# Kernel tuning notes

Measured on AMD Instinct MI355X. Metric: run time of the kernel, lower is better.

Reference implementation:

```python
import jax, jax.numpy as jnp
import numpy as np

B = 1024          # batch
H = 512           # hidden_dim
T = 256           # seq_len
CD = 2            # coord_dim
LAT = 64 + 64 + 128  # total latent dim


def setup_inputs() -> dict:
    key = jax.random.key(0)
    ks = jax.random.split(key, 20)
    s = 0.05  # weight init scale
    rn = lambda k, shp: (jax.random.normal(k, shp, dtype=jnp.float32) * s)
    return {
        "z_primitive": jax.random.normal(ks[0], (B, 64), dtype=jnp.float32),
        "z_skill": jax.random.normal(ks[1], (B, 64), dtype=jnp.float32),
        "z_style": jax.random.normal(ks[2], (B, 128), dtype=jnp.float32),
        "W_proj": rn(ks[3], (2 * H, LAT)),
        "b_proj": jnp.zeros((2 * H,), jnp.float32),
        "Wih1": rn(ks[4], (4 * H, CD)),
        "Whh1": rn(ks[5], (4 * H, H)),
        "bih1": jnp.zeros((4 * H,), jnp.float32),
        "bhh1": jnp.zeros((4 * H,), jnp.float32),
        "Wih2": rn(ks[6], (4 * H, H)),
        "Whh2": rn(ks[7], (4 * H, H)),
        "bih2": jnp.zeros((4 * H,), jnp.float32),
        "bhh2": jnp.zeros((4 * H,), jnp.float32),
        "Wo1": rn(ks[8], (H // 2, H)),
        "bo1": jnp.zeros((H // 2,), jnp.float32),
        "Wo2": rn(ks[9], (CD, H // 2)),
        "bo2": jnp.zeros((CD,), jnp.float32),
    }


def _lstm_cell(x, h, c, Wih, Whh, bih, bhh):
    # PyTorch gate order: i, f, g, o
    gates = x @ Wih.T + h @ Whh.T + (bih + bhh)
    i, f, g, o = jnp.split(gates, 4, axis=1)
    c_new = jax.nn.sigmoid(f) * c + jax.nn.sigmoid(i) * jnp.tanh(g)
    h_new = jax.nn.sigmoid(o) * jnp.tanh(c_new)
    return h_new, c_new


def reference(z_primitive, z_skill, z_style, W_proj, b_proj,
              Wih1, Whh1, bih1, bhh1, Wih2, Whh2, bih2, bhh2,
              Wo1, bo1, Wo2, bo2):
    z = jnp.concatenate([z_primitive, z_skill, z_style], axis=1)  # [B, LAT]
    init = z @ W_proj.T + b_proj                                  # [B, 2H]
    h0 = init[:, :H]
    c0 = init[:, H:]
    x0 = jnp.zeros((z.shape[0], CD), init.dtype)

    def step(carry, _):
        x, h1, c1, h2, c2 = carry
        h1, c1 = _lstm_cell(x, h1, c1, Wih1, Whh1, bih1, bhh1)
        h2, c2 = _lstm_cell(h1, h2, c2, Wih2, Whh2, bih2, bhh2)
        # output MLP (Dropout inactive in eval)
        y = jax.nn.relu(h2 @ Wo1.T + bo1) @ Wo2.T + bo2  # [B, CD]
        return (y, h1, c1, h2, c2), y

    # h0/c0 repeated across both LSTM layers (repeat(2,1,1) in torch)
    _, ys = jax.lax.scan(step, (x0, h0, c0, h0, c0), None, length=T)
    return jnp.transpose(ys, (1, 0, 2))  # [B, T, CD]
```

## Files before the change

kernel.cpp:

```cpp
#include <hip/hip_runtime.h>
#include <math.h>

#define NB 1024
#define NH 512
#define NT 256
#define NCD 2

typedef unsigned short u16;
typedef __bf16 bf16x8 __attribute__((ext_vector_type(8)));
typedef float  f32x4  __attribute__((ext_vector_type(4)));

#define MFMA_BF16 __builtin_amdgcn_mfma_f32_16x16x32_bf16

__device__ __forceinline__ float sigf(float x) { return 1.0f / (1.0f + expf(-x)); }
__device__ __forceinline__ float b2f(u16 u) {
    union { unsigned i; float f; } v; v.i = ((unsigned)u) << 16; return v.f;
}
__device__ __forceinline__ u16 f2b(float f) {
    union { float f; unsigned i; } v; v.f = f;
    unsigned r = v.i + 0x7fffu + ((v.i >> 16) & 1u);
    return (u16)(r >> 16);
}

__device__ __forceinline__ void async_cp16(const void* gptr, void* lptr) {
    __builtin_amdgcn_global_load_lds(
        (const __attribute__((address_space(1))) unsigned int*)gptr,
        (__attribute__((address_space(3))) unsigned int*)lptr,
        16, 0, 0);
}

__global__ __launch_bounds__(256) void convert3(
    const float* __restrict__ a, const float* __restrict__ b,
    const float* __restrict__ c,
    u16* __restrict__ oa, u16* __restrict__ ob, u16* __restrict__ oc)
{
    const int i = blockIdx.x * 256 + threadIdx.x;
    oa[i] = f2b(a[i]); ob[i] = f2b(b[i]); oc[i] = f2b(c[i]);
}

__global__ __launch_bounds__(256) void convw1(
    const float* __restrict__ a, u16* __restrict__ o)
{
    const int i = blockIdx.x * 256 + threadIdx.x;
    o[i] = f2b(a[i]);
}

__global__ __launch_bounds__(256) void bsum_k(
    const float* __restrict__ bi1, const float* __restrict__ bh1,
    const float* __restrict__ bi2, const float* __restrict__ bh2,
    float* __restrict__ o1, float* __restrict__ o2)
{
    const int i = blockIdx.x * 256 + threadIdx.x;
    o1[i] = bi1[i] + bh1[i];
    o2[i] = bi2[i] + bh2[i];
}

__global__ __launch_bounds__(256) void init_kernel(
    const float* __restrict__ zp, const float* __restrict__ zs,
    const float* __restrict__ zst, const float* __restrict__ Wp,
    const float* __restrict__ bp,
    u16* __restrict__ h1, float* __restrict__ c1,
    u16* __restrict__ h2, float* __restrict__ c2)
{
    __shared__ float z[4][256];
    const int tid = threadIdx.x;
    const int b0  = blockIdx.x * 4;
    for (int i = tid; i < 4 * 256; i += 256) {
        const int bb = i >> 8, k = i & 255;
        float v;
        if (k < 64)       v = zp [(b0 + bb) * 64  + k];
        else if (k < 128) v = zs [(b0 + bb) * 64  + (k - 64)];
        else              v = zst[(b0 + bb) * 128 + (k - 128)];
        z[bb][k] = v;
    }
    __syncthreads();
    for (int rt = 0; rt < 4; ++rt) {
        const int r = rt * 256 + tid;
        const float bias = bp[r];
        float a0 = bias, a1 = bias, a2 = bias, a3 = bias;
        for (int k = 0; k < 256; ++k) {
            const float w = Wp[r * 256 + k];
            a0 += z[0][k] * w; a1 += z[1][k] * w;
            a2 += z[2][k] * w; a3 += z[3][k] * w;
        }
        const float acc[4] = {a0, a1, a2, a3};
        for (int bb = 0; bb < 4; ++bb) {
            const int b = b0 + bb;
            if (r < NH) {
                h1[b * NH + r] = f2b(acc[bb]);
                h2[b * NH + r] = f2b(acc[bb]);
            } else {
                c1[b * NH + r - NH] = acc[bb];
                c2[b * NH + r - NH] = acc[bb];
            }
        }
    }
}

__global__ __launch_bounds__(512, 4) void fused_out_lstm1(
    const u16* __restrict__ h2prev,
    const u16* __restrict__ A0,
    const u16* __restrict__ W0,
    const float* __restrict__ bsum,
    const float* __restrict__ Wx,
    const u16* __restrict__ W1b,
    const float* __restrict__ bo1, const float* __restrict__ Wo2,
    const float* __restrict__ bo2, float* __restrict__ outp,
    float* __restrict__ c, u16* __restrict__ hnext,
    const int t, const int do_lstm)
{
    __shared__ __align__(16) char smem[61440];
    float* eg  = (float*)smem;
    float* red = (float*)(smem + 36864);

    const int tid  = threadIdx.x;
    const int lane = tid & 63;
    const int wv   = tid >> 6;
    const int g    = wv & 3;
    const int mh   = wv >> 2;
    const int l15  = lane & 15;
    const int q    = lane >> 4;
    const int bx   = blockIdx.x;
    const int ut   = (bx & 7) * 2 + ((bx >> 3) & 1);
    const int grp  = bx >> 4;
    const int b0   = grp * 32;
    const int u0   = ut * 32;

    int goffW0, goffW1, goffA = 0, goffO[4];
    {
        const int c0 = (wv * 2) * 64 + lane;
        const int w0r = c0 >> 3;
        goffW0 = ((w0r >> 5) * NH + u0 + (w0r & 31)) * NH + (((c0 & 7) ^ (w0r & 7)) * 8);
        const int c1i = (wv * 2 + 1) * 64 + lane;
        const int w1r = c1i >> 3;
        goffW1 = ((w1r >> 5) * NH + u0 + (w1r & 31)) * NH + (((c1i & 7) ^ (w1r & 7)) * 8);
        if (wv < 4) {
            const int ca = wv * 64 + lane;
            const int ar = ca >> 3;
            goffA = (b0 + ar) * NH + (((ca & 7) ^ (ar & 7)) * 8);
        }
#pragma unroll
        for (int i = 0; i < 4; ++i) {
            const int cidx = (wv * 4 + i) * 64 + lane;
            const int row  = cidx >> 3;
            const int kc   = (cidx & 7) ^ (row & 7);
            goffO[i] = row * NH + kc * 8;
        }
    }

    auto issue = [&](int m, int bi) {
        const int k0 = (m & 7) * 64;
        char* base = smem + bi * 20480;
        async_cp16((const void*)(W0 + goffW0 + k0),
                   (void*)(base + 4096 + (wv * 2) * 1024));
        async_cp16((const void*)(W0 + goffW1 + k0),
                   (void*)(base + 4096 + (wv * 2 + 1) * 1024));
        if (wv < 4)
            async_cp16((const void*)(A0 + goffA + k0),
                       (void*)(base + wv * 1024));
    };

    const int u_e  = tid & 31;
    const int bq_e = tid >> 5;
    const int ug_e = u0 + u_e;
    float bs[4], wx0[4], wx1[4], cpre[2];
#pragma unroll
    for (int g4 = 0; g4 < 4; ++g4) bs[g4] = bsum[g4 * NH + ug_e];
#pragma unroll
    for (int g4 = 0; g4 < 4; ++g4) {
        wx0[g4] = Wx[(g4 * NH + ug_e) * 2 + 0];
        wx1[g4] = Wx[(g4 * NH + ug_e) * 2 + 1];
    }
    cpre[0] = c[(size_t)(b0 + bq_e * 2 + 0) * NH + ug_e];
    cpre[1] = c[(size_t)(b0 + bq_e * 2 + 1) * NH + ug_e];

    if (do_lstm) issue(0, 2);

    float r_x[4] = {0.f, 0.f, 0.f, 0.f};

    if (h2prev) {
        f32x4 acc_o[2][2];
#pragma unroll
        for (int mi = 0; mi < 2; ++mi)
#pragma unroll
            for (int ni = 0; ni < 2; ++ni)
                acc_o[mi][ni] = (f32x4){0.f, 0.f, 0.f, 0.f};

        for (int kk = 0; kk < 8; ++kk) {
            __syncthreads();
            const int k0 = kk * 64;
#pragma unroll
            for (int i = 0; i < 4; ++i)
                async_cp16((const void*)(W1b + goffO[i] + k0),
                           (void*)(smem + ((wv * 4 + i) << 10)));
            if (wv < 4)
                async_cp16((const void*)(h2prev + goffA + k0),
                           (void*)(smem + 32768 + (wv << 10)));
            asm volatile("s_waitcnt vmcnt(0)" ::: "memory");
            __builtin_amdgcn_s_barrier();
#pragma unroll
            for (int kh = 0; kh < 2; ++kh) {
                bf16x8 bfr[2], av[2];
#pragma unroll
                for (int ni = 0; ni < 2; ++ni) {
                    const int wrow = wv * 32 + ni * 16 + l15;
                    const int j = (kh * 4 + q) ^ (wrow & 7);
                    bfr[ni] = *(const bf16x8*)(smem + wrow * 128 + j * 16);
                }
#pragma unroll
                for (int mi = 0; mi < 2; ++mi) {
                    const int row = mi * 16 + l15;
                    const int j = (kh * 4 + q) ^ (row & 7);
                    av[mi] = *(const bf16x8*)(smem + 32768 + row * 128 + j * 16);
                }
#pragma unroll
                for (int mi = 0; mi < 2; ++mi)
#pragma unroll
                    for (int ni = 0; ni < 2; ++ni)
                        acc_o[mi][ni] = MFMA_BF16(av[mi], bfr[ni], acc_o[mi][ni], 0, 0, 0);
            }
        }
        float bo1n[2], w20[2], w21[2];
#pragma unroll
        for (int ni = 0; ni < 2; ++ni) {
            const int n = wv * 32 + ni * 16 + l15;
            bo1n[ni] = bo1[n]; w20[ni] = Wo2[n]; w21[ni] = Wo2[256 + n];
        }
        float pa[2][4], pb[2][4];
#pragma unroll
        for (int mi = 0; mi < 2; ++mi)
#pragma unroll
            for (int r = 0; r < 4; ++r) {
                const float s0 = fmaxf(acc_o[mi][0][r] + bo1n[0], 0.f);
                const float s1 = fmaxf(acc_o[mi][1][r] + bo1n[1], 0.f);
                pa[mi][r] = s0 * w20[0] + s1 * w20[1];
                pb[mi][r] = s0 * w21[0] + s1 * w21[1];
            }
#pragma unroll
        for (int off = 1; off < 16; off <<= 1)
#pragma unroll
            for (int mi = 0; mi < 2; ++mi)
#pragma unroll
                for (int r = 0; r < 4; ++r) {
                    pa[mi][r] += __shfl_xor(pa[mi][r], off, 64);
                    pb[mi][r] += __shfl_xor(pb[mi][r], off, 64);
                }
        if (l15 == 0) {
#pragma unroll
            for (int mi = 0; mi < 2; ++mi)
#pragma unroll
                for (int r = 0; r < 4; ++r) {
                    const int m = mi * 16 + q * 4 + r;
                    red[m * 16 + wv * 2 + 0] = pa[mi][r];
                    red[m * 16 + wv * 2 + 1] = pb[mi][r];
                }
        }
        __syncthreads();
        if (ut == 0 && tid < 64) {
            const int bl = tid >> 1, cc = tid & 1;
            float y = bo2[cc];
#pragma unroll
            for (int w8 = 0; w8 < 8; ++w8) y += red[bl * 16 + w8 * 2 + cc];
            outp[(size_t)(b0 + bl) * (NT * NCD) + (t - 1) * NCD + cc] = y;
        }
        if (do_lstm) {
            const int bq = tid >> 5;
#pragma unroll
            for (int jj = 0; jj < 2; ++jj)
#pragma unroll
                for (int cc = 0; cc < 2; ++cc) {
                    float y = bo2[cc];
#pragma unroll
                    for (int w8 = 0; w8 < 8; ++w8)
                        y += red[(bq * 2 + jj) * 16 + w8 * 2 + cc];
                    r_x[jj * 2 + cc] = y;
                }
        }
        __syncthreads();
    }
    if (!do_lstm) return;

    f32x4 acc[2];
    acc[0] = (f32x4){0.f, 0.f, 0.f, 0.f};
    acc[1] = (f32x4){0.f, 0.f, 0.f, 0.f};
    const int M = 8;
    issue(1, 0);
    int ci = 2;
    for (int m = 0; m < M; ++m) {
        if (m + 1 < M) {
            if (wv < 4) asm volatile("s_waitcnt vmcnt(3)" ::: "memory");
            else        asm volatile("s_waitcnt vmcnt(2)" ::: "memory");
        } else {
            asm volatile("s_waitcnt vmcnt(0)" ::: "memory");
        }
        __builtin_amdgcn_s_barrier();
        if (m + 2 < M) {
            int bi = ci + 2; if (bi >= 3) bi -= 3;
            issue(m + 2, bi);
        }
        const char* bA = smem + ci * 20480;
        const char* bW = bA + 4096;
#pragma unroll
        for (int khi = 0; khi < 2; ++khi) {
            bf16x8 bfr[2];
#pragma unroll
            for (int ni = 0; ni < 2; ++ni) {
                const int wrow = g * 32 + ni * 16 + l15;
                const int j = (khi * 4 + q) ^ (wrow & 7);
                bfr[ni] = *(const bf16x8*)(bW + wrow * 128 + j * 16);
            }
            const int row = mh * 16 + l15;
            const int j = (khi * 4 + q) ^ (row & 7);
            const bf16x8 av = *(const bf16x8*)(bA + row * 128 + j * 16);
            acc[0] = MFMA_BF16(av, bfr[0], acc[0], 0, 0, 0);
            acc[1] = MFMA_BF16(av, bfr[1], acc[1], 0, 0, 0);
        }
        ++ci; if (ci == 3) ci = 0;
    }

    __syncthreads();
#pragma unroll
    for (int ni = 0; ni < 2; ++ni)
#pragma unroll
        for (int r = 0; r < 4; ++r)
            eg[(g * 32 + mh * 16 + q * 4 + r) * 33 + ni * 16 + l15] = acc[ni][r];
    __syncthreads();

#pragma unroll
    for (int jj = 0; jj < 2; ++jj) {
        const int bl = bq_e * 2 + jj;
        const int b  = b0 + bl;
        float gv[4];
#pragma unroll
        for (int g4 = 0; g4 < 4; ++g4) gv[g4] = eg[(g4 * 32 + bl) * 33 + u_e] + bs[g4];
        const float x0 = r_x[jj * 2 + 0];
        const float x1 = r_x[jj * 2 + 1];
#pragma unroll
        for (int g4 = 0; g4 < 4; ++g4) gv[g4] += x0 * wx0[g4] + x1 * wx1[g4];
        const float iv = sigf(gv[0]);
        const float fv = sigf(gv[1]);
        const float gg = tanhf(gv[2]);
        const float ov = sigf(gv[3]);
        const size_t idx = (size_t)b * NH + ug_e;
        const float cn = fv * cpre[jj] + iv * gg;
        c[idx] = cn;
        hnext[idx] = f2b(ov * tanhf(cn));
    }
}

__global__ __launch_bounds__(512, 4) void lstm_mfma32(
    const u16* __restrict__ A0, const u16* __restrict__ W0,
    const u16* __restrict__ A1, const u16* __restrict__ W1,
    const float* __restrict__ bsum,
    float* __restrict__ c, u16* __restrict__ hnext,
    const int npass)
{
    __shared__ __align__(16) char smem[61440];
    float* eg = (float*)smem;

    const int tid  = threadIdx.x;
    const int lane = tid & 63;
    const int wv   = tid >> 6;
    const int g    = wv & 3;
    const int mh   = wv >> 2;
    const int l15  = lane & 15;
    const int q    = lane >> 4;
    const int bx   = blockIdx.x;
    const int ut   = (bx & 7) * 2 + ((bx >> 3) & 1);
    const int grp  = bx >> 4;
    const int b0   = grp * 32;
    const int u0   = ut * 32;

    int goffW0, goffW1, goffA = 0;
    {
        const int c0 = (wv * 2) * 64 + lane;
        const int w0r = c0 >> 3;
        goffW0 = ((w0r >> 5) * NH + u0 + (w0r & 31)) * NH + (((c0 & 7) ^ (w0r & 7)) * 8);
        const int c1i = (wv * 2 + 1) * 64 + lane;
        const int w1r = c1i >> 3;
        goffW1 = ((w1r >> 5) * NH + u0 + (w1r & 31)) * NH + (((c1i & 7) ^ (w1r & 7)) * 8);
        if (wv < 4) {
            const int ca = wv * 64 + lane;
            const int ar = ca >> 3;
            goffA = (b0 + ar) * NH + (((ca & 7) ^ (ar & 7)) * 8);
        }
    }

    const int u_e  = tid & 31;
    const int bq_e = tid >> 5;
    const int ug_e = u0 + u_e;
    float bs[4], cpre[2];
#pragma unroll
    for (int g4 = 0; g4 < 4; ++g4) bs[g4] = bsum[g4 * NH + ug_e];
    cpre[0] = c[(size_t)(b0 + bq_e * 2 + 0) * NH + ug_e];
    cpre[1] = c[(size_t)(b0 + bq_e * 2 + 1) * NH + ug_e];

    f32x4 acc[2];
    acc[0] = (f32x4){0.f, 0.f, 0.f, 0.f};
    acc[1] = (f32x4){0.f, 0.f, 0.f, 0.f};

    const int M = npass * 8;

    auto issue = [&](int m, int bi) {
        const u16* __restrict__ Ap = (m < 8) ? A0 : A1;
        const u16* __restrict__ Wp = (m < 8) ? W0 : W1;
        const int k0 = (m & 7) * 64;
        char* base = smem + bi * 20480;
        async_cp16((const void*)(Wp + goffW0 + k0),
                   (void*)(base + 4096 + (wv * 2) * 1024));
        async_cp16((const void*)(Wp + goffW1 + k0),
                   (void*)(base + 4096 + (wv * 2 + 1) * 1024));
        if (wv < 4)
            async_cp16((const void*)(Ap + goffA + k0),
                       (void*)(base + wv * 1024));
    };

    issue(0, 0);
    if (M > 1) issue(1, 1);
    int ci = 0;
    for (int m = 0; m < M; ++m) {
        if (m + 1 < M) {
            if (wv < 4) asm volatile("s_waitcnt vmcnt(3)" ::: "memory");
            else        asm volatile("s_waitcnt vmcnt(2)" ::: "memory");
        } else {
            asm volatile("s_waitcnt vmcnt(0)" ::: "memory");
        }
        __builtin_amdgcn_s_barrier();
        if (m + 2 < M) {
            int bi = ci + 2; if (bi >= 3) bi -= 3;
            issue(m + 2, bi);
        }
        const char* bA = smem + ci * 20480;
        const char* bW = bA + 4096;
#pragma unroll
        for (int khi = 0; khi < 2; ++khi) {
            bf16x8 bfr[2];
#pragma unroll
            for (int ni = 0; ni < 2; ++ni) {
                const int wrow = g * 32 + ni * 16 + l15;
                const int j = (khi * 4 + q) ^ (wrow & 7);
                bfr[ni] = *(const bf16x8*)(bW + wrow * 128 + j * 16);
            }
            const int row = mh * 16 + l15;
            const int j = (khi * 4 + q) ^ (row & 7);
            const bf16x8 av = *(const bf16x8*)(bA + row * 128 + j * 16);
            acc[0] = MFMA_BF16(av, bfr[0], acc[0], 0, 0, 0);
            acc[1] = MFMA_BF16(av, bfr[1], acc[1], 0, 0, 0);
        }
        ++ci; if (ci == 3) ci = 0;
    }

    __syncthreads();
#pragma unroll
    for (int ni = 0; ni < 2; ++ni)
#pragma unroll
        for (int r = 0; r < 4; ++r)
            eg[(g * 32 + mh * 16 + q * 4 + r) * 33 + ni * 16 + l15] = acc[ni][r];
    __syncthreads();

#pragma unroll
    for (int jj = 0; jj < 2; ++jj) {
        const int bl = bq_e * 2 + jj;
        const int b  = b0 + bl;
        float gv[4];
#pragma unroll
        for (int g4 = 0; g4 < 4; ++g4) gv[g4] = eg[(g4 * 32 + bl) * 33 + u_e] + bs[g4];
        const float iv = sigf(gv[0]);
        const float fv = sigf(gv[1]);
        const float gg = tanhf(gv[2]);
        const float ov = sigf(gv[3]);
        const size_t idx = (size_t)b * NH + ug_e;
        const float cn = fv * cpre[jj] + iv * gg;
        c[idx] = cn;
        hnext[idx] = f2b(ov * tanhf(cn));
    }
}

extern "C" void kernel_launch(void* const* d_in, const int* in_sizes, int n_in,
                              void* d_out, int out_size, void* d_ws, size_t ws_size,
                              hipStream_t stream)
{
    const float* zp   = (const float*)d_in[0];
    const float* zsk  = (const float*)d_in[1];
    const float* zst  = (const float*)d_in[2];
    const float* Wp   = (const float*)d_in[3];
    const float* bp   = (const float*)d_in[4];
    const float* Wih1 = (const float*)d_in[5];
    const float* Whh1 = (const float*)d_in[6];
    const float* bih1 = (const float*)d_in[7];
    const float* bhh1 = (const float*)d_in[8];
    const float* Wih2 = (const float*)d_in[9];
    const float* Whh2 = (const float*)d_in[10];
    const float* bih2 = (const float*)d_in[11];
    const float* bhh2 = (const float*)d_in[12];
    const float* Wo1  = (const float*)d_in[13];
    const float* bo1  = (const float*)d_in[14];
    const float* Wo2  = (const float*)d_in[15];
    const float* bo2  = (const float*)d_in[16];

    const size_t BH = (size_t)NB * NH;
    u16*   h1a   = (u16*)d_ws;
    u16*   h1b   = h1a + BH;
    u16*   h2a   = h1b + BH;
    u16*   h2b   = h2a + BH;
    float* c1    = (float*)(h2b + BH);
    float* c2    = c1 + BH;
    float* bs1   = c2 + BH;
    float* bs2   = bs1 + 2048;
    u16*   Wo1b  = (u16*)(bs2 + 2048);
    u16*   Whh1b = Wo1b + 131072;
    u16*   Wih2b = Whh1b + 1048576;
    u16*   Whh2b = Wih2b + 1048576;

    convert3<<<(2048 * 512) / 256, 256, 0, stream>>>(Whh1, Wih2, Whh2, Whh1b, Wih2b, Whh2b);
    convw1<<<(256 * 512) / 256, 256, 0, stream>>>(Wo1, Wo1b);
    bsum_k<<<2048 / 256, 256, 0, stream>>>(bih1, bhh1, bih2, bhh2, bs1, bs2);
    init_kernel<<<NB / 4, 256, 0, stream>>>(zp, zsk, zst, Wp, bp, h1a, c1, h2a, c2);

    u16* h1c = h1a; u16* h1n = h1b;
    u16* h2c = h2a; u16* h2n = h2b;
    float* outp = (float*)d_out;
    for (int t = 0; t < NT; ++t) {
        fused_out_lstm1<<<512, 512, 0, stream>>>(
            (t == 0) ? (const u16*)0 : h2c, h1c, Whh1b, bs1, Wih1,
            Wo1b, bo1, Wo2, bo2, outp, c1, h1n, t, 1);
        lstm_mfma32<<<512, 512, 0, stream>>>(h1n, Wih2b, h2c, Whh2b,
                                             bs2, c2, h2n, 2);
        u16* tmp = h1c; h1c = h1n; h1n = tmp;
        tmp = h2c; h2c = h2n; h2n = tmp;
    }
    fused_out_lstm1<<<512, 512, 0, stream>>>(
        h2c, h1c, Whh1b, bs1, Wih1,
        Wo1b, bo1, Wo2, bo2, outp, c1, h1n, NT, 0);
}
```

Measured before the change: 7.488 ms.

## Fuse both LSTM layers per step using a per-batch-group atomic barrier

Merges the layer-2 LSTM kernel into the layer-1/output kernel. The 16 blocks sharing a batch group synchronise through an atomic counter barrier in global memory before layer 2 reads h1. Layer 2 loads the h1/h2 activations with relaxed atomic register loads and writes them to LDS, while the weights still use async global-to-LDS copies. This removes one kernel launch per timestep and its launch/drain gap. It depends on all 512 blocks being co-resident, and the spin loop has a guard cap that could silently proceed without full synchronisation.

```diff
diff --git a/kernel.cpp b/kernel.cpp
--- a/kernel.cpp
+++ b/kernel.cpp
@@ -9,13 +9,11 @@
 typedef unsigned short u16;
 typedef __bf16 bf16x8 __attribute__((ext_vector_type(8)));
 typedef float  f32x4  __attribute__((ext_vector_type(4)));
+typedef unsigned int  u32x4 __attribute__((ext_vector_type(4)));
 
 #define MFMA_BF16 __builtin_amdgcn_mfma_f32_16x16x32_bf16
 
 __device__ __forceinline__ float sigf(float x) { return 1.0f / (1.0f + expf(-x)); }
-__device__ __forceinline__ float b2f(u16 u) {
-    union { unsigned i; float f; } v; v.i = ((unsigned)u) << 16; return v.f;
-}
 __device__ __forceinline__ u16 f2b(float f) {
     union { float f; unsigned i; } v; v.f = f;
     unsigned r = v.i + 0x7fffu + ((v.i >> 16) & 1u);
@@ -29,6 +27,16 @@
         16, 0, 0);
 }
 
+__device__ __forceinline__ u32x4 aload16(const u16* p) {
+    unsigned* q = (unsigned*)(void*)p;
+    u32x4 v;
+    v.x = __hip_atomic_load(q + 0, __ATOMIC_RELAXED, __HIP_MEMORY_SCOPE_AGENT);
+    v.y = __hip_atomic_load(q + 1, __ATOMIC_RELAXED, __HIP_MEMORY_SCOPE_AGENT);
+    v.z = __hip_atomic_load(q + 2, __ATOMIC_RELAXED, __HIP_MEMORY_SCOPE_AGENT);
+    v.w = __hip_atomic_load(q + 3, __ATOMIC_RELAXED, __HIP_MEMORY_SCOPE_AGENT);
+    return v;
+}
+
 __global__ __launch_bounds__(256) void convert3(
     const float* __restrict__ a, const float* __restrict__ b,
     const float* __restrict__ c,
@@ -53,6 +61,11 @@
     const int i = blockIdx.x * 256 + threadIdx.x;
     o1[i] = bi1[i] + bh1[i];
     o2[i] = bi2[i] + bh2[i];
+}
+
+__global__ __launch_bounds__(512) void zero_bar(unsigned* __restrict__ b)
+{
+    b[threadIdx.x] = 0u;
 }
 
 __global__ __launch_bounds__(256) void init_kernel(
@@ -97,16 +110,21 @@
     }
 }
 
-__global__ __launch_bounds__(512, 4) void fused_out_lstm1(
+__global__ __launch_bounds__(512, 4) void step_fused(
     const u16* __restrict__ h2prev,
     const u16* __restrict__ A0,
     const u16* __restrict__ W0,
-    const float* __restrict__ bsum,
+    const float* __restrict__ bsum1,
     const float* __restrict__ Wx,
     const u16* __restrict__ W1b,
     const float* __restrict__ bo1, const float* __restrict__ Wo2,
     const float* __restrict__ bo2, float* __restrict__ outp,
-    float* __restrict__ c, u16* __restrict__ hnext,
+    float* __restrict__ c1, u16* __restrict__ h1next,
+    const u16* __restrict__ Wih2b, const u16* __restrict__ Whh2b,
+    const float* __restrict__ bsum2,
+    float* __restrict__ c2, const u16* __restrict__ h2cur,
+    u16* __restrict__ h2next,
+    unsigned* bar,
     const int t, const int do_lstm)
 {
     __shared__ __align__(16) char smem[61440];
@@ -159,20 +177,31 @@
             async_cp16((const void*)(A0 + goffA + k0),
                        (void*)(base + wv * 1024));
     };
+    auto issueW2 = [&](const u16* Wp, int m, int bi) {
+        const int k0 = (m & 7) * 64;
+        char* base = smem + bi * 20480;
+        async_cp16((const void*)(Wp + goffW0 + k0), (void*)(base + 4096 + (wv * 2) * 1024));
+        async_cp16((const void*)(Wp + goffW1 + k0), (void*)(base + 4096 + (wv * 2 + 1) * 1024));
+    };
+    auto awrite = [&](char* base, u32x4 v) {
+        *(u32x4*)(base + wv * 1024 + lane * 16) = v;
+    };
 
     const int u_e  = tid & 31;
     const int bq_e = tid >> 5;
     const int ug_e = u0 + u_e;
-    float bs[4], wx0[4], wx1[4], cpre[2];
-#pragma unroll
-    for (int g4 = 0; g4 < 4; ++g4) bs[g4] = bsum[g4 * NH + ug_e];
+    float bs1r[4], bs2r[4], wx0[4], wx1[4], c1pre[2], c2pre[2];
 #pragma unroll
     for (int g4 = 0; g4 < 4; ++g4) {
-        wx0[g4] = Wx[(g4 * NH + ug_e) * 2 + 0];
-        wx1[g4] = Wx[(g4 * NH + ug_e) * 2 + 1];
-    }
-    cpre[0] = c[(size_t)(b0 + bq_e * 2 + 0) * NH + ug_e];
-    cpre[1] = c[(size_t)(b0 + bq_e * 2 + 1) * NH + ug_e];
+        bs1r[g4] = bsum1[g4 * NH + ug_e];
+        bs2r[g4] = bsum2[g4 * NH + ug_e];
+        wx0[g4]  = Wx[(g4 * NH + ug_e) * 2 + 0];
+        wx1[g4]  = Wx[(g4 * NH + ug_e) * 2 + 1];
+    }
+    c1pre[0] = c1[(size_t)(b0 + bq_e * 2 + 0) * NH + ug_e];
+    c1pre[1] = c1[(size_t)(b0 + bq_e * 2 + 1) * NH + ug_e];
+    c2pre[0] = c2[(size_t)(b0 + bq_e * 2 + 0) * NH + ug_e];
+    c2pre[1] = c2[(size_t)(b0 + bq_e * 2 + 1) * NH + ug_e];
 
     if (do_lstm) issue(0, 2);
 
@@ -264,7 +293,6 @@
             outp[(size_t)(b0 + bl) * (NT * NCD) + (t - 1) * NCD + cc] = y;
         }
         if (do_lstm) {
-            const int bq = tid >> 5;
 #pragma unroll
             for (int jj = 0; jj < 2; ++jj)
 #pragma unroll
@@ -272,7 +300,7 @@
                     float y = bo2[cc];
 #pragma unroll
                     for (int w8 = 0; w8 < 8; ++w8)
-                        y += red[(bq * 2 + jj) * 16 + w8 * 2 + cc];
+                        y += red[(bq_e * 2 + jj) * 16 + w8 * 2 + cc];
                     r_x[jj * 2 + cc] = y;
                 }
         }
@@ -280,199 +308,173 @@
     }
     if (!do_lstm) return;
 
-    f32x4 acc[2];
-    acc[0] = (f32x4){0.f, 0.f, 0.f, 0.f};
-    acc[1] = (f32x4){0.f, 0.f, 0.f, 0.f};
-    const int M = 8;
-    issue(1, 0);
-    int ci = 2;
-    for (int m = 0; m < M; ++m) {
-        if (m + 1 < M) {
-            if (wv < 4) asm volatile("s_waitcnt vmcnt(3)" ::: "memory");
-            else        asm volatile("s_waitcnt vmcnt(2)" ::: "memory");
-        } else {
-            asm volatile("s_waitcnt vmcnt(0)" ::: "memory");
-        }
-        __builtin_amdgcn_s_barrier();
-        if (m + 2 < M) {
-            int bi = ci + 2; if (bi >= 3) bi -= 3;
-            issue(m + 2, bi);
-        }
-        const char* bA = smem + ci * 20480;
-        const char* bW = bA + 4096;
-#pragma unroll
-        for (int khi = 0; khi < 2; ++khi) {
-            bf16x8 bfr[2];
-#pragma unroll
-            for (int ni = 0; ni < 2; ++ni) {
-                const int wrow = g * 32 + ni * 16 + l15;
-                const int j = (khi * 4 + q) ^ (wrow & 7);
-                bfr[ni] = *(const bf16x8*)(bW + wrow * 128 + j * 16);
-            }
-            const int row = mh * 16 + l15;
-            const int j = (khi * 4 + q) ^ (row & 7);
-            const bf16x8 av = *(const bf16x8*)(bA + row * 128 + j * 16);
-            acc[0] = MFMA_BF16(av, bfr[0], acc[0], 0, 0, 0);
-            acc[1] = MFMA_BF16(av, bfr[1], acc[1], 0, 0, 0);
-        }
-        ++ci; if (ci == 3) ci = 0;
-    }
-
-    __syncthreads();
-#pragma unroll
-    for (int ni = 0; ni < 2; ++ni)
-#pragma unroll
-        for (int r = 0; r < 4; ++r)
-            eg[(g * 32 + mh * 16 + q * 4 + r) * 33 + ni * 16 + l15] = acc[ni][r];
-    __syncthreads();
-
-#pragma unroll
-    for (int jj = 0; jj < 2; ++jj) {
-        const int bl = bq_e * 2 + jj;
-        const int b  = b0 + bl;
-        float gv[4];
-#pragma unroll
-        for (int g4 = 0; g4 < 4; ++g4) gv[g4] = eg[(g4 * 32 + bl) * 33 + u_e] + bs[g4];
-        const float x0 = r_x[jj * 2 + 0];
-        const float x1 = r_x[jj * 2 + 1];
-#pragma unroll
-        for (int g4 = 0; g4 < 4; ++g4) gv[g4] += x0 * wx0[g4] + x1 * wx1[g4];
-        const float iv = sigf(gv[0]);
-        const float fv = sigf(gv[1]);
-        const float gg = tanhf(gv[2]);
-        const float ov = sigf(gv[3]);
-        const size_t idx = (size_t)b * NH + ug_e;
-        const float cn = fv * cpre[jj] + iv * gg;
-        c[idx] = cn;
-        hnext[idx] = f2b(ov * tanhf(cn));
-    }
-}
-
-__global__ __launch_bounds__(512, 4) void lstm_mfma32(
-    const u16* __restrict__ A0, const u16* __restrict__ W0,
-    const u16* __restrict__ A1, const u16* __restrict__ W1,
-    const float* __restrict__ bsum,
-    float* __restrict__ c, u16* __restrict__ hnext,
-    const int npass)
-{
-    __shared__ __align__(16) char smem[61440];
-    float* eg = (float*)smem;
-
-    const int tid  = threadIdx.x;
-    const int lane = tid & 63;
-    const int wv   = tid >> 6;
-    const int g    = wv & 3;
-    const int mh   = wv >> 2;
-    const int l15  = lane & 15;
-    const int q    = lane >> 4;
-    const int bx   = blockIdx.x;
-    const int ut   = (bx & 7) * 2 + ((bx >> 3) & 1);
-    const int grp  = bx >> 4;
-    const int b0   = grp * 32;
-    const int u0   = ut * 32;
-
-    int goffW0, goffW1, goffA = 0;
     {
-        const int c0 = (wv * 2) * 64 + lane;
-        const int w0r = c0 >> 3;
-        goffW0 = ((w0r >> 5) * NH + u0 + (w0r & 31)) * NH + (((c0 & 7) ^ (w0r & 7)) * 8);
-        const int c1i = (wv * 2 + 1) * 64 + lane;
-        const int w1r = c1i >> 3;
-        goffW1 = ((w1r >> 5) * NH + u0 + (w1r & 31)) * NH + (((c1i & 7) ^ (w1r & 7)) * 8);
+        f32x4 acc[2];
+        acc[0] = (f32x4){0.f, 0.f, 0.f, 0.f};
+        acc[1] = (f32x4){0.f, 0.f, 0.f, 0.f};
+        const int M = 8;
+        issue(1, 0);
+        int ci = 2;
+        for (int m = 0; m < M; ++m) {
+            if (m + 1 < M) {
+                if (wv < 4) asm volatile("s_waitcnt vmcnt(3)" ::: "memory");
+                else        asm volatile("s_waitcnt vmcnt(2)" ::: "memory");
+            } else {
+                asm volatile("s_waitcnt vmcnt(0)" ::: "memory");
+            }
+            __builtin_amdgcn_s_barrier();
+            if (m + 2 < M) {
+                int bi = ci + 2; if (bi >= 3) bi -= 3;
+                issue(m + 2, bi);
+            }
+            const char* bA = smem + ci * 20480;
+            const char* bW = bA + 4096;
+#pragma unroll
+            for (int khi = 0; khi < 2; ++khi) {
+                bf16x8 bfr[2];
+#pragma unroll
+                for (int ni = 0; ni < 2; ++ni) {
+                    const int wrow = g * 32 + ni * 16 + l15;
+                    const int j = (khi * 4 + q) ^ (wrow & 7);
+                    bfr[ni] = *(const bf16x8*)(bW + wrow * 128 + j * 16);
+                }
+                const int row = mh * 16 + l15;
+                const int j = (khi * 4 + q) ^ (row & 7);
+                const bf16x8 av = *(const bf16x8*)(bA + row * 128 + j * 16);
+                acc[0] = MFMA_BF16(av, bfr[0], acc[0], 0, 0, 0);
+                acc[1] = MFMA_BF16(av, bfr[1], acc[1], 0, 0, 0);
+            }
+            ++ci; if (ci == 3) ci = 0;
+        }
+
+        __syncthreads();
+#pragma unroll
+        for (int ni = 0; ni < 2; ++ni)
+#pragma unroll
+            for (int r = 0; r < 4; ++r)
+                eg[(g * 32 + mh * 16 + q * 4 + r) * 33 + ni * 16 + l15] = acc[ni][r];
+        __syncthreads();
+
+#pragma unroll
+        for (int jj = 0; jj < 2; ++jj) {
+            const int bl = bq_e * 2 + jj;
+            const int b  = b0 + bl;
+            float gv[4];
+#pragma unroll
+            for (int g4 = 0; g4 < 4; ++g4) gv[g4] = eg[(g4 * 32 + bl) * 33 + u_e] + bs1r[g4];
+            const float x0 = r_x[jj * 2 + 0];
+            const float x1 = r_x[jj * 2 + 1];
+#pragma unroll
+            for (int g4 = 0; g4 < 4; ++g4) gv[g4] += x0 * wx0[g4] + x1 * wx1[g4];
+            const float iv = sigf(gv[0]);
+            const float fv = sigf(gv[1]);
+            const float gg = tanhf(gv[2]);
+            const float ov = sigf(gv[3]);
+            const size_t idx = (size_t)b * NH + ug_e;
+            const float cn = fv * c1pre[jj] + iv * gg;
+            c1[idx] = cn;
+            const unsigned hb = (unsigned)f2b(ov * tanhf(cn));
+            const unsigned pr = (unsigned)__shfl_xor((int)hb, 1, 64);
+            if (!(u_e & 1))
+                __hip_atomic_store((unsigned*)(void*)(h1next + idx),
+                                   hb | (pr << 16),
+                                   __ATOMIC_RELAXED, __HIP_MEMORY_SCOPE_AGENT);
+        }
+    }
+
+    {
+        unsigned* mybar = bar + grp * 16;
+        const unsigned target = 16u * (unsigned)(t + 1);
+        __syncthreads();
+        if (tid == 0) {
+            __hip_atomic_fetch_add(mybar, 1u, __ATOMIC_RELAXED, __HIP_MEMORY_SCOPE_AGENT);
+            int guard = 0;
+            while (__hip_atomic_load(mybar, __ATOMIC_RELAXED, __HIP_MEMORY_SCOPE_AGENT)
+                       < target && ++guard < (1 << 20)) {
+                __builtin_amdgcn_s_sleep(1);
+            }
+        }
+        __syncthreads();
+    }
+
+    {
+        f32x4 acc[2];
+        acc[0] = (f32x4){0.f, 0.f, 0.f, 0.f};
+        acc[1] = (f32x4){0.f, 0.f, 0.f, 0.f};
+        u32x4 rB0, rB1;
+        if (wv < 4) rB0 = aload16(h1next + goffA);
+        issueW2(Wih2b, 0, 0);
+        if (wv < 4) rB1 = aload16(h1next + goffA + 64);
+        issueW2(Wih2b, 1, 1);
         if (wv < 4) {
-            const int ca = wv * 64 + lane;
-            const int ar = ca >> 3;
-            goffA = (b0 + ar) * NH + (((ca & 7) ^ (ar & 7)) * 8);
-        }
-    }
-
-    const int u_e  = tid & 31;
-    const int bq_e = tid >> 5;
-    const int ug_e = u0 + u_e;
-    float bs[4], cpre[2];
-#pragma unroll
-    for (int g4 = 0; g4 < 4; ++g4) bs[g4] = bsum[g4 * NH + ug_e];
-    cpre[0] = c[(size_t)(b0 + bq_e * 2 + 0) * NH + ug_e];
-    cpre[1] = c[(size_t)(b0 + bq_e * 2 + 1) * NH + ug_e];
-
-    f32x4 acc[2];
-    acc[0] = (f32x4){0.f, 0.f, 0.f, 0.f};
-    acc[1] = (f32x4){0.f, 0.f, 0.f, 0.f};
-
-    const int M = npass * 8;
-
-    auto issue = [&](int m, int bi) {
-        const u16* __restrict__ Ap = (m < 8) ? A0 : A1;
-        const u16* __restrict__ Wp = (m < 8) ? W0 : W1;
-        const int k0 = (m & 7) * 64;
-        char* base = smem + bi * 20480;
-        async_cp16((const void*)(Wp + goffW0 + k0),
-                   (void*)(base + 4096 + (wv * 2) * 1024));
-        async_cp16((const void*)(Wp + goffW1 + k0),
-                   (void*)(base + 4096 + (wv * 2 + 1) * 1024));
-        if (wv < 4)
-            async_cp16((const void*)(Ap + goffA + k0),
-                       (void*)(base + wv * 1024));
-    };
-
-    issue(0, 0);
-    if (M > 1) issue(1, 1);
-    int ci = 0;
-    for (int m = 0; m < M; ++m) {
-        if (m + 1 < M) {
-            if (wv < 4) asm volatile("s_waitcnt vmcnt(3)" ::: "memory");
-            else        asm volatile("s_waitcnt vmcnt(2)" ::: "memory");
-        } else {
-            asm volatile("s_waitcnt vmcnt(0)" ::: "memory");
-        }
-        __builtin_amdgcn_s_barrier();
-        if (m + 2 < M) {
-            int bi = ci + 2; if (bi >= 3) bi -= 3;
-            issue(m + 2, bi);
-        }
-        const char* bA = smem + ci * 20480;
-        const char* bW = bA + 4096;
-#pragma unroll
-        for (int khi = 0; khi < 2; ++khi) {
-            bf16x8 bfr[2];
-#pragma unroll
-            for (int ni = 0; ni < 2; ++ni) {
-                const int wrow = g * 32 + ni * 16 + l15;
-                const int j = (khi * 4 + q) ^ (wrow & 7);
-                bfr[ni] = *(const bf16x8*)(bW + wrow * 128 + j * 16);
-            }
-            const int row = mh * 16 + l15;
-            const int j = (khi * 4 + q) ^ (row & 7);
-            const bf16x8 av = *(const bf16x8*)(bA + row * 128 + j * 16);
-            acc[0] = MFMA_BF16(av, bfr[0], acc[0], 0, 0, 0);
-            acc[1] = MFMA_BF16(av, bfr[1], acc[1], 0, 0, 0);
-        }
-        ++ci; if (ci == 3) ci = 0;
-    }
-
-    __syncthreads();
-#pragma unroll
-    for (int ni = 0; ni < 2; ++ni)
-#pragma unroll
-        for (int r = 0; r < 4; ++r)
-            eg[(g * 32 + mh * 16 + q * 4 + r) * 33 + ni * 16 + l15] = acc[ni][r];
-    __syncthreads();
-
-#pragma unroll
-    for (int jj = 0; jj < 2; ++jj) {
-        const int bl = bq_e * 2 + jj;
-        const int b  = b0 + bl;
-        float gv[4];
-#pragma unroll
-        for (int g4 = 0; g4 < 4; ++g4) gv[g4] = eg[(g4 * 32 + bl) * 33 + u_e] + bs[g4];
-        const float iv = sigf(gv[0]);
-        const float fv = sigf(gv[1]);
-        const float gg = tanhf(gv[2]);
-        const float ov = sigf(gv[3]);
-        const size_t idx = (size_t)b * NH + ug_e;
-        const float cn = fv * cpre[jj] + iv * gg;
-        c[idx] = cn;
-        hnext[idx] = f2b(ov * tanhf(cn));
+            awrite(smem + 0 * 20480, rB0);
+            awrite(smem + 1 * 20480, rB1);
+            rB0 = aload16(h1next + goffA + 128);
+        }
+        int ci = 0;
+        for (int m = 0; m < 16; ++m) {
+            if (m + 1 < 16) {
+                if (wv < 4) asm volatile("s_waitcnt vmcnt(6) lgkmcnt(0)" ::: "memory");
+                else        asm volatile("s_waitcnt vmcnt(2)" ::: "memory");
+            } else {
+                asm volatile("s_waitcnt vmcnt(0) lgkmcnt(0)" ::: "memory");
+            }
+            __builtin_amdgcn_s_barrier();
+            if (m + 2 < 16) {
+                int bi = ci + 2; if (bi >= 3) bi -= 3;
+                if (wv < 4) awrite(smem + bi * 20480, (m & 1) ? rB1 : rB0);
+                issueW2((m + 2 < 8) ? Wih2b : Whh2b, m + 2, bi);
+                if (wv < 4 && m + 3 < 16) {
+                    const u16* Ap = (m + 3 < 8) ? h1next : h2cur;
+                    const int k0 = ((m + 3) & 7) * 64;
+                    if (m & 1) rB0 = aload16(Ap + goffA + k0);
+                    else       rB1 = aload16(Ap + goffA + k0);
+                }
+            }
+            const char* bA = smem + ci * 20480;
+            const char* bW = bA + 4096;
+#pragma unroll
+            for (int khi = 0; khi < 2; ++khi) {
+                bf16x8 bfr[2];
+#pragma unroll
+                for (int ni = 0; ni < 2; ++ni) {
+                    const int wrow = g * 32 + ni * 16 + l15;
+                    const int j = (khi * 4 + q) ^ (wrow & 7);
+                    bfr[ni] = *(const bf16x8*)(bW + wrow * 128 + j * 16);
+                }
+                const int row = mh * 16 + l15;
+                const int j = (khi * 4 + q) ^ (row & 7);
+                const bf16x8 av = *(const bf16x8*)(bA + row * 128 + j * 16);
+                acc[0] = MFMA_BF16(av, bfr[0], acc[0], 0, 0, 0);
+                acc[1] = MFMA_BF16(av, bfr[1], acc[1], 0, 0, 0);
+            }
+            ++ci; if (ci == 3) ci = 0;
+        }
+
+        __syncthreads();
+#pragma unroll
+        for (int ni = 0; ni < 2; ++ni)
+#pragma unroll
+            for (int r = 0; r < 4; ++r)
+                eg[(g * 32 + mh * 16 + q * 4 + r) * 33 + ni * 16 + l15] = acc[ni][r];
+        __syncthreads();
+
+#pragma unroll
+        for (int jj = 0; jj < 2; ++jj) {
+            const int bl = bq_e * 2 + jj;
+            const int b  = b0 + bl;
+            float gv[4];
+#pragma unroll
+            for (int g4 = 0; g4 < 4; ++g4) gv[g4] = eg[(g4 * 32 + bl) * 33 + u_e] + bs2r[g4];
+            const float iv = sigf(gv[0]);
+            const float fv = sigf(gv[1]);
+            const float gg = tanhf(gv[2]);
+            const float ov = sigf(gv[3]);
+            const size_t idx = (size_t)b * NH + ug_e;
+            const float cn = fv * c2pre[jj] + iv * gg;
+            c2[idx] = cn;
+            h2next[idx] = f2b(ov * tanhf(cn));
+        }
     }
 }
 
@@ -511,25 +513,27 @@
     u16*   Whh1b = Wo1b + 131072;
     u16*   Wih2b = Whh1b + 1048576;
     u16*   Whh2b = Wih2b + 1048576;
+    unsigned* bar = (unsigned*)(Whh2b + 1048576);
 
     convert3<<<(2048 * 512) / 256, 256, 0, stream>>>(Whh1, Wih2, Whh2, Whh1b, Wih2b, Whh2b);
     convw1<<<(256 * 512) / 256, 256, 0, stream>>>(Wo1, Wo1b);
     bsum_k<<<2048 / 256, 256, 0, stream>>>(bih1, bhh1, bih2, bhh2, bs1, bs2);
     init_kernel<<<NB / 4, 256, 0, stream>>>(zp, zsk, zst, Wp, bp, h1a, c1, h2a, c2);
+    zero_bar<<<1, 512, 0, stream>>>(bar);
 
     u16* h1c = h1a; u16* h1n = h1b;
     u16* h2c = h2a; u16* h2n = h2b;
     float* outp = (float*)d_out;
     for (int t = 0; t < NT; ++t) {
-        fused_out_lstm1<<<512, 512, 0, stream>>>(
+        step_fused<<<512, 512, 0, stream>>>(
             (t == 0) ? (const u16*)0 : h2c, h1c, Whh1b, bs1, Wih1,
-            Wo1b, bo1, Wo2, bo2, outp, c1, h1n, t, 1);
-        lstm_mfma32<<<512, 512, 0, stream>>>(h1n, Wih2b, h2c, Whh2b,
-                                             bs2, c2, h2n, 2);
+            Wo1b, bo1, Wo2, bo2, outp, c1, h1n,
+            Wih2b, Whh2b, bs2, c2, h2c, h2n, bar, t, 1);
         u16* tmp = h1c; h1c = h1n; h1n = tmp;
         tmp = h2c; h2c = h2n; h2n = tmp;
     }
-    fused_out_lstm1<<<512, 512, 0, stream>>>(
+    step_fused<<<512, 512, 0, stream>>>(
         h2c, h1c, Whh1b, bs1, Wih1,
-        Wo1b, bo1, Wo2, bo2, outp, c1, h1n, NT, 0);
-}
+        Wo1b, bo1, Wo2, bo2, outp, c1, h1n,
+        Wih2b, Whh2b, bs2, c2, h2c, h2n, bar, NT, 0);
+}
```

Measured after the change: 8.335 ms. 1.11x slower.

## Split output MLP across unit-tile blocks and combine via atomics and group barrier

Applied to the files above, without the earlier changes.

Previously every block computed the full Wo1 output layer (all 256 hidden units) for its 32-row batch group, which duplicated the work across the 16 unit-tile blocks of that group. Now each block computes only a 16-unit slice and atomically adds its partial output into the output buffer. A spin barrier per batch group then lets blocks read back the completed y as the next input x. This removes the 16x redundant MLP compute and Wo1 loads. In exchange it adds atomics, a cross-block spin wait that depends on all 16 blocks being co-resident, and summation order that is not deterministic.

```diff
diff --git a/kernel.cpp b/kernel.cpp
--- a/kernel.cpp
+++ b/kernel.cpp
@@ -13,9 +13,6 @@
 #define MFMA_BF16 __builtin_amdgcn_mfma_f32_16x16x32_bf16
 
 __device__ __forceinline__ float sigf(float x) { return 1.0f / (1.0f + expf(-x)); }
-__device__ __forceinline__ float b2f(u16 u) {
-    union { unsigned i; float f; } v; v.i = ((unsigned)u) << 16; return v.f;
-}
 __device__ __forceinline__ u16 f2b(float f) {
     union { float f; unsigned i; } v; v.f = f;
     unsigned r = v.i + 0x7fffu + ((v.i >> 16) & 1u);
@@ -29,6 +26,10 @@
         16, 0, 0);
 }
 
+__device__ __forceinline__ float aloadf(const float* p) {
+    return __hip_atomic_load((float*)p, __ATOMIC_RELAXED, __HIP_MEMORY_SCOPE_AGENT);
+}
+
 __global__ __launch_bounds__(256) void convert3(
     const float* __restrict__ a, const float* __restrict__ b,
     const float* __restrict__ c,
@@ -53,6 +54,16 @@
     const int i = blockIdx.x * 256 + threadIdx.x;
     o1[i] = bi1[i] + bh1[i];
     o2[i] = bi2[i] + bh2[i];
+}
+
+__global__ __launch_bounds__(512) void zero_bar(unsigned* __restrict__ b)
+{
+    b[threadIdx.x] = 0u;
+}
+
+__global__ __launch_bounds__(512) void zero_out(float* __restrict__ o)
+{
+    o[blockIdx.x * 512 + threadIdx.x] = 0.f;
 }
 
 __global__ __launch_bounds__(256) void init_kernel(
@@ -107,11 +118,11 @@
     const float* __restrict__ bo1, const float* __restrict__ Wo2,
     const float* __restrict__ bo2, float* __restrict__ outp,
     float* __restrict__ c, u16* __restrict__ hnext,
+    unsigned* __restrict__ bar,
     const int t, const int do_lstm)
 {
     __shared__ __align__(16) char smem[61440];
     float* eg  = (float*)smem;
-    float* red = (float*)(smem + 36864);
 
     const int tid  = threadIdx.x;
     const int lane = tid & 63;
@@ -126,7 +137,7 @@
     const int b0   = grp * 32;
     const int u0   = ut * 32;
 
-    int goffW0, goffW1, goffA = 0, goffO[4];
+    int goffW0, goffW1, goffA = 0, goffWS = 0;
     {
         const int c0 = (wv * 2) * 64 + lane;
         const int w0r = c0 >> 3;
@@ -139,12 +150,10 @@
             const int ar = ca >> 3;
             goffA = (b0 + ar) * NH + (((ca & 7) ^ (ar & 7)) * 8);
         }
-#pragma unroll
-        for (int i = 0; i < 4; ++i) {
-            const int cidx = (wv * 4 + i) * 64 + lane;
-            const int row  = cidx >> 3;
-            const int kc   = (cidx & 7) ^ (row & 7);
-            goffO[i] = row * NH + kc * 8;
+        if (wv == 4 || wv == 5) {
+            const int cs = (wv - 4) * 64 + lane;
+            const int rl = cs >> 3;
+            goffWS = (ut * 16 + rl) * NH + (((cs & 7) ^ (rl & 7)) * 8);
         }
     }
 
@@ -176,65 +185,45 @@
 
     if (do_lstm) issue(0, 2);
 
-    float r_x[4] = {0.f, 0.f, 0.f, 0.f};
-
     if (h2prev) {
-        f32x4 acc_o[2][2];
-#pragma unroll
-        for (int mi = 0; mi < 2; ++mi)
-#pragma unroll
-            for (int ni = 0; ni < 2; ++ni)
-                acc_o[mi][ni] = (f32x4){0.f, 0.f, 0.f, 0.f};
+        f32x4 acc_o[2];
+        acc_o[0] = (f32x4){0.f, 0.f, 0.f, 0.f};
+        acc_o[1] = (f32x4){0.f, 0.f, 0.f, 0.f};
 
         for (int kk = 0; kk < 8; ++kk) {
             __syncthreads();
             const int k0 = kk * 64;
-#pragma unroll
-            for (int i = 0; i < 4; ++i)
-                async_cp16((const void*)(W1b + goffO[i] + k0),
-                           (void*)(smem + ((wv * 4 + i) << 10)));
             if (wv < 4)
                 async_cp16((const void*)(h2prev + goffA + k0),
                            (void*)(smem + 32768 + (wv << 10)));
+            if (wv == 4 || wv == 5)
+                async_cp16((const void*)(W1b + goffWS + k0),
+                           (void*)(smem + 36864 + ((wv - 4) << 10)));
             asm volatile("s_waitcnt vmcnt(0)" ::: "memory");
             __builtin_amdgcn_s_barrier();
 #pragma unroll
             for (int kh = 0; kh < 2; ++kh) {
-                bf16x8 bfr[2], av[2];
-#pragma unroll
-                for (int ni = 0; ni < 2; ++ni) {
-                    const int wrow = wv * 32 + ni * 16 + l15;
-                    const int j = (kh * 4 + q) ^ (wrow & 7);
-                    bfr[ni] = *(const bf16x8*)(smem + wrow * 128 + j * 16);
+                const int j = (kh * 4 + q) ^ (l15 & 7);
+                const bf16x8 bfr = *(const bf16x8*)(smem + 36864 + l15 * 128 + j * 16);
+#pragma unroll
+                for (int mi = 0; mi < 2; ++mi) {
+                    const bf16x8 av = *(const bf16x8*)(smem + 32768 + (mi * 16 + l15) * 128 + j * 16);
+                    acc_o[mi] = MFMA_BF16(av, bfr, acc_o[mi], 0, 0, 0);
                 }
-#pragma unroll
-                for (int mi = 0; mi < 2; ++mi) {
-                    const int row = mi * 16 + l15;
-                    const int j = (kh * 4 + q) ^ (row & 7);
-                    av[mi] = *(const bf16x8*)(smem + 32768 + row * 128 + j * 16);
-                }
-#pragma unroll
-                for (int mi = 0; mi < 2; ++mi)
-#pragma unroll
-                    for (int ni = 0; ni < 2; ++ni)
-                        acc_o[mi][ni] = MFMA_BF16(av[mi], bfr[ni], acc_o[mi][ni], 0, 0, 0);
             }
         }
-        float bo1n[2], w20[2], w21[2];
-#pragma unroll
-        for (int ni = 0; ni < 2; ++ni) {
-            const int n = wv * 32 + ni * 16 + l15;
-            bo1n[ni] = bo1[n]; w20[ni] = Wo2[n]; w21[ni] = Wo2[256 + n];
-        }
+        const int ng = ut * 16 + l15;
+        const float bo1n = bo1[ng];
+        const float w20  = Wo2[ng];
+        const float w21  = Wo2[256 + ng];
         float pa[2][4], pb[2][4];
 #pragma unroll
         for (int mi = 0; mi < 2; ++mi)
 #pragma unroll
             for (int r = 0; r < 4; ++r) {
-                const float s0 = fmaxf(acc_o[mi][0][r] + bo1n[0], 0.f);
-                const float s1 = fmaxf(acc_o[mi][1][r] + bo1n[1], 0.f);
-                pa[mi][r] = s0 * w20[0] + s1 * w20[1];
-                pb[mi][r] = s0 * w21[0] + s1 * w21[1];
+                const float s = fmaxf(acc_o[mi][r] + bo1n, 0.f);
+                pa[mi][r] = s * w20;
+                pb[mi][r] = s * w21;
             }
 #pragma unroll
         for (int off = 1; off < 16; off <<= 1)
@@ -245,35 +234,17 @@
                     pa[mi][r] += __shfl_xor(pa[mi][r], off, 64);
                     pb[mi][r] += __shfl_xor(pb[mi][r], off, 64);
                 }
-        if (l15 == 0) {
+        if (wv == 0 && l15 == 0) {
+            const float b20 = (ut == 0) ? bo2[0] : 0.f;
+            const float b21 = (ut == 0) ? bo2[1] : 0.f;
 #pragma unroll
             for (int mi = 0; mi < 2; ++mi)
 #pragma unroll
                 for (int r = 0; r < 4; ++r) {
                     const int m = mi * 16 + q * 4 + r;
-                    red[m * 16 + wv * 2 + 0] = pa[mi][r];
-                    red[m * 16 + wv * 2 + 1] = pb[mi][r];
-                }
-        }
-        __syncthreads();
-        if (ut == 0 && tid < 64) {
-            const int bl = tid >> 1, cc = tid & 1;
-            float y = bo2[cc];
-#pragma unroll
-            for (int w8 = 0; w8 < 8; ++w8) y += red[bl * 16 + w8 * 2 + cc];
-            outp[(size_t)(b0 + bl) * (NT * NCD) + (t - 1) * NCD + cc] = y;
-        }
-        if (do_lstm) {
-            const int bq = tid >> 5;
-#pragma unroll
-            for (int jj = 0; jj < 2; ++jj)
-#pragma unroll
-                for (int cc = 0; cc < 2; ++cc) {
-                    float y = bo2[cc];
-#pragma unroll
-                    for (int w8 = 0; w8 < 8; ++w8)
-                        y += red[(bq * 2 + jj) * 16 + w8 * 2 + cc];
-                    r_x[jj * 2 + cc] = y;
+                    float* dst = outp + (size_t)(b0 + m) * (NT * NCD) + (t - 1) * NCD;
+                    atomicAdd(dst + 0, pa[mi][r] + b20);
+                    atomicAdd(dst + 1, pb[mi][r] + b21);
                 }
         }
         __syncthreads();
@@ -316,6 +287,29 @@
             acc[1] = MFMA_BF16(av, bfr[1], acc[1], 0, 0, 0);
         }
         ++ci; if (ci == 3) ci = 0;
+    }
+
+    float r_x[4] = {0.f, 0.f, 0.f, 0.f};
+    if (h2prev) {
+        unsigned* mybar = bar + grp * 16;
+        const unsigned target = 16u * (unsigned)t;
+        __syncthreads();
+        if (tid == 0) {
+            __hip_atomic_fetch_add(mybar, 1u, __ATOMIC_RELAXED, __HIP_MEMORY_SCOPE_AGENT);
+            int guard = 0;
+            while (__hip_atomic_load(mybar, __ATOMIC_RELAXED, __HIP_MEMORY_SCOPE_AGENT)
+                       < target && ++guard < (1 << 20)) {
+                __builtin_amdgcn_s_sleep(1);
+            }
+        }
+        __syncthreads();
+#pragma unroll
+        for (int jj = 0; jj < 2; ++jj) {
+            const float* src = outp + (size_t)(b0 + bq_e * 2 + jj) * (NT * NCD)
+                               + (t - 1) * NCD;
+            r_x[jj * 2 + 0] = aloadf(src + 0);
+            r_x[jj * 2 + 1] = aloadf(src + 1);
+        }
     }
 
     __syncthreads();
@@ -511,11 +505,14 @@
     u16*   Whh1b = Wo1b + 131072;
     u16*   Wih2b = Whh1b + 1048576;
     u16*   Whh2b = Wih2b + 1048576;
+    unsigned* bar = (unsigned*)(Whh2b + 1048576);
 
     convert3<<<(2048 * 512) / 256, 256, 0, stream>>>(Whh1, Wih2, Whh2, Whh1b, Wih2b, Whh2b);
     convw1<<<(256 * 512) / 256, 256, 0, stream>>>(Wo1, Wo1b);
     bsum_k<<<2048 / 256, 256, 0, stream>>>(bih1, bhh1, bih2, bhh2, bs1, bs2);
     init_kernel<<<NB / 4, 256, 0, stream>>>(zp, zsk, zst, Wp, bp, h1a, c1, h2a, c2);
+    zero_bar<<<1, 512, 0, stream>>>(bar);
+    zero_out<<<(NB * NT * NCD) / 512, 512, 0, stream>>>((float*)d_out);
 
     u16* h1c = h1a; u16* h1n = h1b;
     u16* h2c = h2a; u16* h2n = h2b;
@@ -523,7 +520,7 @@
     for (int t = 0; t < NT; ++t) {
         fused_out_lstm1<<<512, 512, 0, stream>>>(
             (t == 0) ? (const u16*)0 : h2c, h1c, Whh1b, bs1, Wih1,
-            Wo1b, bo1, Wo2, bo2, outp, c1, h1n, t, 1);
+            Wo1b, bo1, Wo2, bo2, outp, c1, h1n, bar, t, 1);
         lstm_mfma32<<<512, 512, 0, stream>>>(h1n, Wih2b, h2c, Whh2b,
                                              bs2, c2, h2n, 2);
         u16* tmp = h1c; h1c = h1n; h1n = tmp;
@@ -531,5 +528,5 @@
     }
     fused_out_lstm1<<<512, 512, 0, stream>>>(
         h2c, h1c, Whh1b, bs1, Wih1,
-        Wo1b, bo1, Wo2, bo2, outp, c1, h1n, NT, 0);
-}
+        Wo1b, bo1, Wo2, bo2, outp, c1, h1n, bar, NT, 0);
+}
```

Result: no change. 7.436 ms (-0.7%).
